# Kernel tuning notes

Measured on AMD Instinct MI355X. Metric: run time of the kernel, lower is better.

Reference implementation:

```python
import jax, jax.numpy as jnp
import numpy as np

B, N, DEG = 32, 1024, 8
E = B * N * DEG
NT = B * N
F_IN, HID, EDIM, NR, HD = 64, 128, 16, 16, 4
NEG = 0.2  # leaky_relu negative slope (alpha)
K1 = int(np.ceil(0.8 * N))    # 820 kept nodes per graph after pool1
K2 = int(np.ceil(0.8 * K1))   # 656 kept nodes per graph after pool2


def setup_inputs() -> dict:
    key = jax.random.key(0)
    ks = jax.random.split(key, 20)
    nrm = lambda i, shp, s=0.05: jax.random.normal(ks[i], shp, jnp.float32) * s
    x = jax.random.normal(ks[0], (NT, F_IN), jnp.float32)
    off = (jnp.arange(B) * N)[:, None]
    src = (jax.random.randint(ks[1], (B, N * DEG), 0, N) + off).reshape(-1)
    dst = (jax.random.randint(ks[2], (B, N * DEG), 0, N) + off).reshape(-1)
    edge_index = jnp.stack([src, dst]).astype(jnp.int32)
    edge_attr = jax.random.normal(ks[3], (E, EDIM), jnp.float32)
    action = jax.random.normal(ks[4], (B, NR), jnp.float32)
    return dict(
        x=x, edge_attr=edge_attr, action=action,
        W1l=nrm(5, (F_IN, HD * HID)), b1l=jnp.zeros(HD * HID),
        W1r=nrm(6, (F_IN, HD * HID)), b1r=jnp.zeros(HD * HID),
        W1e=nrm(7, (EDIM, HD * HID)), att1=nrm(8, (HD, HID)), bias1=jnp.zeros(HID),
        W2l=nrm(9, (HID, HD * HID)), b2l=jnp.zeros(HD * HID),
        W2r=nrm(10, (HID, HD * HID)), b2r=jnp.zeros(HD * HID),
        W2e=nrm(11, (EDIM, HD * HID)), att2=nrm(12, (HD, HID)), bias2=jnp.zeros(HID),
        p1=nrm(13, (HID,), 0.1), p2=nrm(14, (HID,), 0.1),
        Wf1=nrm(15, (2 * HID + NR, HID)), bf1=jnp.zeros(HID),
        Wf2=nrm(16, (HID, HID)), bf2=jnp.zeros(HID),
        Wf3=nrm(17, (HID, 1), 0.003), bf3=jnp.zeros(1),
        edge_index=edge_index,
    )


def _gatv2(x, edge_index, edge_attr, edge_mask, Wl, bl, Wr, br, We, att, bias):
    # PyG GATv2Conv, concat=False (mean over heads), eval mode (no dropout).
    src, dst = edge_index[0], edge_index[1]
    n = x.shape[0]
    xl = (x @ Wl + bl).reshape(n, HD, HID)   # source transform (x_j)
    xr = (x @ Wr + br).reshape(n, HD, HID)   # target transform (x_i)
    ef = (edge_attr @ We).reshape(-1, HD, HID)
    m = jax.nn.leaky_relu(xl[src] + xr[dst] + ef, NEG)          # [E,H,C]
    logits = jnp.where(edge_mask[:, None], (m * att).sum(-1), -1e9)  # [E,H]
    mx = jax.ops.segment_max(logits, dst, num_segments=n)
    a = jnp.exp(logits - mx[dst])
    den = jax.ops.segment_sum(a, dst, num_segments=n)
    alpha = (a / (den[dst] + 1e-16)) * edge_mask[:, None]       # softmax per dst, masked edges zeroed
    out = jax.ops.segment_sum(xl[src] * alpha[..., None], dst, num_segments=n)
    return out.mean(axis=1) + bias


def _topk(x, node_mask, p, k):
    # PyG TopKPooling: score = x@p/||p||, gate = tanh(score), keep top-k per graph.
    score = (x @ p) / (jnp.linalg.norm(p) + 1e-16)
    gate = jnp.tanh(score)
    s = jnp.where(node_mask, score, -jnp.inf).reshape(B, N)
    idx = jax.lax.top_k(s, k)[1]                                # [B,k]
    keep = jnp.zeros((B, N), bool).at[jnp.arange(B)[:, None], idx].set(True).reshape(-1)
    return x * gate[:, None], keep


def reference(x, edge_attr, action, W1l, b1l, W1r, b1r, W1e, att1, bias1,
              W2l, b2l, W2r, b2r, W2e, att2, bias2, p1, p2,
              Wf1, bf1, Wf2, bf2, Wf3, bf3, edge_index):
    src, dst = edge_index[0], edge_index[1]
    em0 = jnp.ones((E,), bool)
    h = jax.nn.relu(_gatv2(x, edge_index, edge_attr, em0,
                           W1l, b1l, W1r, b1r, W1e, att1, bias1))
    h, keep1 = _topk(h, jnp.ones((NT,), bool), p1, K1)
    em1 = keep1[src] & keep1[dst]
    h = jax.nn.relu(_gatv2(h, edge_index, edge_attr, em1,
                           W2l, b2l, W2r, b2r, W2e, att2, bias2))
    h, keep2 = _topk(h, keep1, p2, K2)
    hb = h.reshape(B, N, HID)
    mb = keep2.reshape(B, N)[..., None]
    gmx = jnp.where(mb, hb, -jnp.inf).max(axis=1)               # global max pool over kept nodes
    gav = (hb * mb).sum(axis=1) / K2                            # global mean pool (K2 kept per graph)
    z = jnp.concatenate([gmx, gav, action], axis=1)             # [B, 2*HID+NR]
    z = jax.nn.relu(z @ Wf1 + bf1)
    z = jax.nn.relu(z @ Wf2 + bf2)
    return z @ Wf3 + bf3
```

## Files before the change

kernel.cpp:

```cpp
#include <hip/hip_runtime.h>
#include <math.h>

#define NTN 32768
#define NBG 32
#define NN  1024
#define EPG 8192
#define EE  262144
#define FIN 64
#define HIDC 128
#define HD  4
#define HC  512
#define EDIM 16
#define NR  16
#define KP1 820
#define KP2 656
#define NKEPT (KP1 * NBG)
#define NEGS 0.2f
#define NPB 2
#define SHIFT 10.0f

template<int K>
__global__ __launch_bounds__(256) void gemm_node3(const float* __restrict__ A,
                                                  const float* __restrict__ Wl,
                                                  const float* __restrict__ bl,
                                                  const float* __restrict__ Wr,
                                                  const float* __restrict__ br,
                                                  const float* __restrict__ gs,
                                                  const int* __restrict__ ids,
                                                  float* __restrict__ Cl,
                                                  float* __restrict__ Cr,
                                                  const int* __restrict__ perm,
                                                  const float* __restrict__ ea,
                                                  float* __restrict__ eaP) {
    __shared__ float a_s[64][K];
    __shared__ int rid_s[64];
    __shared__ float g_s[64];
    int t = threadIdx.x;
    int rb = blockIdx.x >> 2, cg = blockIdx.x & 3;
    int row0 = rb * 64;
    if (t < 64) {
        int rid = ids ? ids[row0 + t] : (row0 + t);
        rid_s[t] = rid;
        g_s[t] = gs ? tanhf(gs[rid]) : 1.0f;
    }
    __syncthreads();
    for (int i = t; i < 64 * K; i += 256) {
        int r = i / K, k = i % K;
        a_s[r][k] = A[(size_t)rid_s[r] * K + k] * g_s[r];
    }
    __syncthreads();
    int tc = cg * 128 + (t & 63) * 2;
    int rg = (t >> 6) * 16;
    float accl0[16], accl1[16], accr0[16], accr1[16];
    float2 blv = *(const float2*)&bl[tc];
    float2 brv = *(const float2*)&br[tc];
    #pragma unroll
    for (int r = 0; r < 16; r++) { accl0[r] = blv.x; accl1[r] = blv.y; accr0[r] = brv.x; accr1[r] = brv.y; }
    for (int k = 0; k < K; k++) {
        float2 wl = *(const float2*)&Wl[(size_t)k * HC + tc];
        float2 wr = *(const float2*)&Wr[(size_t)k * HC + tc];
        #pragma unroll
        for (int r = 0; r < 16; r++) {
            float a = a_s[rg + r][k];
            accl0[r] += a * wl.x; accl1[r] += a * wl.y;
            accr0[r] += a * wr.x; accr1[r] += a * wr.y;
        }
    }
    for (int r = 0; r < 16; r++) {
        size_t base = (size_t)rid_s[rg + r] * HC + tc;
        *(float2*)&Cl[base] = make_float2(accl0[r], accl1[r]);
        *(float2*)&Cr[base] = make_float2(accr0[r], accr1[r]);
    }
    if (perm) {
        int ng = gridDim.x * 256;
        for (int p = blockIdx.x * 256 + t; p < EE; p += ng) {
            int e = perm[p];
            const float4* s4 = (const float4*)(ea + (size_t)e * EDIM);
            float4* d4 = (float4*)(eaP + (size_t)p * EDIM);
            d4[0] = s4[0]; d4[1] = s4[1]; d4[2] = s4[2]; d4[3] = s4[3];
        }
    }
}

__global__ __launch_bounds__(1024) void csr_build(const int* __restrict__ dst,
                                                  const int* __restrict__ src,
                                                  int* __restrict__ off,
                                                  int* __restrict__ esrc,
                                                  int* __restrict__ perm,
                                                  const float* __restrict__ p1,
                                                  const float* __restrict__ p2,
                                                  float* __restrict__ pn) {
    int g = blockIdx.x, t = threadIdx.x;
    __shared__ int degS[NN];
    __shared__ int scanS[NN];
    __shared__ int curS[NN];
    degS[t] = 0;
    __syncthreads();
    int eb = g * EPG;
    #pragma unroll
    for (int i = t; i < EPG; i += 1024) atomicAdd(&degS[dst[eb + i] - g * NN], 1);
    __syncthreads();
    int dg = degS[t];
    scanS[t] = dg;
    for (int o = 1; o < NN; o <<= 1) {
        __syncthreads();
        int v = (t >= o) ? scanS[t - o] : 0;
        __syncthreads();
        scanS[t] += v;
    }
    __syncthreads();
    int excl = scanS[t] - dg;
    off[g * NN + t] = eb + excl;
    curS[t] = excl;
    if (g == NBG - 1 && t == NN - 1) off[NTN] = EE;
    if (g == 0 && t < 64) {
        float a = p1[t] * p1[t] + p1[t + 64] * p1[t + 64];
        float b = p2[t] * p2[t] + p2[t + 64] * p2[t + 64];
        #pragma unroll
        for (int sft = 32; sft; sft >>= 1) { a += __shfl_xor(a, sft, 64); b += __shfl_xor(b, sft, 64); }
        if (t == 0) { pn[0] = 1.f / (sqrtf(a) + 1e-16f); pn[1] = 1.f / (sqrtf(b) + 1e-16f); }
    }
    __syncthreads();
    #pragma unroll
    for (int i = t; i < EPG; i += 1024) {
        int e = eb + i;
        int ld = dst[e] - g * NN;
        int p = eb + atomicAdd(&curS[ld], 1);
        esrc[p] = src[e];
        perm[p] = e;
    }
}

template<bool L2>
__global__ __launch_bounds__(256, 4) void gat_dst(
        const float* __restrict__ xl, const float* __restrict__ xr,
        const float* __restrict__ eaP, const float* __restrict__ We,
        const float* __restrict__ att, const float* __restrict__ bias,
        const float* __restrict__ pvec, const float* __restrict__ pnInv,
        const int* __restrict__ esrc, const int* __restrict__ off,
        const int* __restrict__ dlist,
        float* __restrict__ out, float* __restrict__ score, int nblk) {
    int bid = blockIdx.x;
    int swz = (bid & 7) * (nblk >> 3) + (bid >> 3);
    int d0 = swz * NPB;
    int t = threadIdx.x;
    int w = t >> 6, lane = t & 63;
    int c = w * HIDC + lane * 2;
    __shared__ float red[NPB][HC];
    __shared__ float red2[NPB][HIDC];
    float we0[EDIM], we1[EDIM];
    #pragma unroll
    for (int k = 0; k < EDIM; k++) {
        we0[k] = We[k * HC + c];
        we1[k] = We[k * HC + c + 1];
    }
    float at0 = att[c], at1 = att[c + 1];

    for (int n = 0; n < NPB; n++) {
        int d = L2 ? dlist[d0 + n] : (d0 + n);
        float denA = 0.f, aA0 = 0.f, aA1 = 0.f;
        float denB = 0.f, aB0 = 0.f, aB1 = 0.f;
        {
            float2 xrv = *(const float2*)&xr[((size_t)d << 9) + c];
            int e0 = off[d], e1 = off[d + 1];
            int ei = e0;
            for (; ei + 4 <= e1; ei += 4) {
                int s[4]; float mk[4]; float2 xv[4]; float p[4];
                #pragma unroll
                for (int j = 0; j < 4; j++) {
                    int sv = esrc[ei + j];
                    if (L2) {
                        mk[j] = sv >= 0 ? 1.f : 0.f;
                        s[j] = sv >= 0 ? sv : 0;
                    } else {
                        s[j] = sv;
                    }
                }
                #pragma unroll
                for (int j = 0; j < 4; j++) xv[j] = *(const float2*)&xl[((size_t)s[j] << 9) + c];
                #pragma unroll
                for (int j = 0; j < 4; j++) {
                    const float4* eap = (const float4*)(eaP + ((size_t)(ei + j) << 4));
                    float4 E0 = eap[0], E1 = eap[1], E2 = eap[2], E3 = eap[3];
                    float ev[16] = {E0.x, E0.y, E0.z, E0.w, E1.x, E1.y, E1.z, E1.w,
                                    E2.x, E2.y, E2.z, E2.w, E3.x, E3.y, E3.z, E3.w};
                    float ef0 = 0.f, ef1 = 0.f;
                    #pragma unroll
                    for (int k = 0; k < EDIM; k++) { ef0 += ev[k] * we0[k]; ef1 += ev[k] * we1[k]; }
                    float v0 = xv[j].x + xrv.x + ef0; v0 = v0 > 0.f ? v0 : NEGS * v0;
                    float v1 = xv[j].y + xrv.y + ef1; v1 = v1 > 0.f ? v1 : NEGS * v1;
                    p[j] = v0 * at0 + v1 * at1;
                }
                #pragma unroll
                for (int sft = 32; sft; sft >>= 1) {
                    #pragma unroll
                    for (int j = 0; j < 4; j++) p[j] += __shfl_xor(p[j], sft, 64);
                }
                float w0 = __expf(p[0] - SHIFT);
                float w1 = __expf(p[1] - SHIFT);
                float w2 = __expf(p[2] - SHIFT);
                float w3 = __expf(p[3] - SHIFT);
                if (L2) { w0 *= mk[0]; w1 *= mk[1]; w2 *= mk[2]; w3 *= mk[3]; }
                denA += w0; aA0 += w0 * xv[0].x; aA1 += w0 * xv[0].y;
                denB += w1; aB0 += w1 * xv[1].x; aB1 += w1 * xv[1].y;
                denA += w2; aA0 += w2 * xv[2].x; aA1 += w2 * xv[2].y;
                denB += w3; aB0 += w3 * xv[3].x; aB1 += w3 * xv[3].y;
            }
            for (; ei < e1; ei++) {
                int sv = esrc[ei];
                float mk = 1.f;
                int s = sv;
                if (L2) { mk = sv >= 0 ? 1.f : 0.f; s = sv >= 0 ? sv : 0; }
                const float4* eap = (const float4*)(eaP + ((size_t)ei << 4));
                float4 E0 = eap[0], E1 = eap[1], E2 = eap[2], E3 = eap[3];
                float2 xv = *(const float2*)&xl[((size_t)s << 9) + c];
                float ev[16] = {E0.x, E0.y, E0.z, E0.w, E1.x, E1.y, E1.z, E1.w,
                                E2.x, E2.y, E2.z, E2.w, E3.x, E3.y, E3.z, E3.w};
                float ef0 = 0.f, ef1 = 0.f;
                #pragma unroll
                for (int k = 0; k < EDIM; k++) { ef0 += ev[k] * we0[k]; ef1 += ev[k] * we1[k]; }
                float v0 = xv.x + xrv.x + ef0; v0 = v0 > 0.f ? v0 : NEGS * v0;
                float v1 = xv.y + xrv.y + ef1; v1 = v1 > 0.f ? v1 : NEGS * v1;
                float p = v0 * at0 + v1 * at1;
                #pragma unroll
                for (int sft = 32; sft; sft >>= 1) p += __shfl_xor(p, sft, 64);
                float wt = __expf(p - SHIFT);
                if (L2) wt *= mk;
                denA += wt; aA0 += wt * xv.x; aA1 += wt * xv.y;
            }
        }
        float inv = 1.f / (denA + denB + 1e-16f);
        red[n][c] = (aA0 + aB0) * inv;
        red[n][c + 1] = (aA1 + aB1) * inv;
    }
    __syncthreads();
    {
        int n2 = t >> 7, tc = t & 127;
        int dd = L2 ? dlist[d0 + n2] : (d0 + n2);
        float v = (red[n2][tc] + red[n2][tc + 128] + red[n2][tc + 256] + red[n2][tc + 384]) * 0.25f
                  + bias[tc];
        v = fmaxf(v, 0.f);
        out[((size_t)dd << 7) + tc] = v;
        red2[n2][tc] = v * pvec[tc];
    }
    __syncthreads();
    if (t < 128) {
        int n3 = t >> 6, l2 = t & 63;
        float sv = red2[n3][l2] + red2[n3][l2 + 64];
        #pragma unroll
        for (int sft = 32; sft; sft >>= 1) sv += __shfl_xor(sv, sft, 64);
        if (l2 == 0) {
            int dd = L2 ? dlist[d0 + n3] : (d0 + n3);
            score[dd] = sv * pnInv[0];
        }
    }
}

__global__ __launch_bounds__(512) void topk_sel(const float* __restrict__ score,
                                                const int* __restrict__ mask, int k,
                                                int* __restrict__ keep, int* __restrict__ klist,
                                                const int* __restrict__ esrc,
                                                int* __restrict__ esrc2) {
    __shared__ float v[NN];
    __shared__ short id[NN];
    __shared__ char kpS[NN];
    int g = blockIdx.x, t = threadIdx.x;
    for (int i = t; i < NN; i += 512) {
        int n = g * NN + i;
        bool mk = mask ? (mask[n] != 0) : true;
        v[i] = mk ? score[n] : -INFINITY;
        id[i] = (short)i;
    }
    __syncthreads();
    for (int kk = 2; kk <= NN; kk <<= 1) {
        for (int j = kk >> 1; j > 0; j >>= 1) {
            #pragma unroll 2
            for (int i = t; i < NN; i += 512) {
                int ixj = i ^ j;
                if (ixj > i) {
                    bool up = ((i & kk) == 0);
                    float a = v[i], b2 = v[ixj];
                    short ia = id[i], ib = id[ixj];
                    bool aFirst = (a > b2) || (a == b2 && ia < ib);
                    if (up ? !aFirst : aFirst) { v[i] = b2; v[ixj] = a; id[i] = ib; id[ixj] = ia; }
                }
            }
            __syncthreads();
        }
    }
    for (int i = t; i < NN; i += 512) {
        int kp = (i < k) ? 1 : 0;
        keep[g * NN + id[i]] = kp;
        kpS[id[i]] = (char)kp;
        if (klist && kp) klist[g * k + i] = g * NN + id[i];
    }
    __syncthreads();
    if (esrc2) {
        int eb = g * EPG;
        for (int i = t; i < EPG; i += 512) {
            int sv = esrc[eb + i];
            esrc2[eb + i] = kpS[sv - g * NN] ? sv : -1;
        }
    }
}

__global__ __launch_bounds__(512) void tail(const float* __restrict__ score,
                                            const int* __restrict__ mask,
                                            const float* __restrict__ h,
                                            const float* __restrict__ action,
                                            const float* __restrict__ Wf1, const float* __restrict__ bf1,
                                            const float* __restrict__ Wf2, const float* __restrict__ bf2,
                                            const float* __restrict__ Wf3, const float* __restrict__ bf3,
                                            float* __restrict__ out) {
    int g = blockIdx.x, t = threadIdx.x;
    __shared__ float v[NN];
    __shared__ short id[NN];
    __shared__ float gt_s[NN];
    __shared__ char kp_s[NN];
    __shared__ float smx[4][HIDC], ssm[4][HIDC];
    __shared__ float zs[2 * HIDC + NR], z1[HIDC], z2[HIDC], rr[HIDC];
    for (int i = t; i < NN; i += 512) {
        int n = g * NN + i;
        bool mk = (mask[n] != 0);
        v[i] = mk ? score[n] : -INFINITY;
        id[i] = (short)i;
        kp_s[i] = 0;
        gt_s[i] = 0.f;
    }
    __syncthreads();
    for (int kk = 2; kk <= NN; kk <<= 1) {
        for (int j = kk >> 1; j > 0; j >>= 1) {
            #pragma unroll 2
            for (int i = t; i < NN; i += 512) {
                int ixj = i ^ j;
                if (ixj > i) {
                    bool up = ((i & kk) == 0);
                    float a = v[i], b2 = v[ixj];
                    short ia = id[i], ib = id[ixj];
                    bool aFirst = (a > b2) || (a == b2 && ia < ib);
                    if (up ? !aFirst : aFirst) { v[i] = b2; v[ixj] = a; id[i] = ib; id[ixj] = ia; }
                }
            }
            __syncthreads();
        }
    }
    for (int i = t; i < NN; i += 512) {
        if (i < KP2) {
            int nid = id[i];
            kp_s[nid] = 1;
            gt_s[nid] = tanhf(score[g * NN + nid]);
        }
    }
    __syncthreads();
    int c = t & 127, ch = t >> 7;
    float mx = -INFINITY, sm = 0.f;
    for (int n = ch * 256; n < ch * 256 + 256; n++) {
        if (kp_s[n]) {
            float hv = h[(size_t)(g * NN + n) * HIDC + c] * gt_s[n];
            mx = fmaxf(mx, hv);
            sm += hv;
        }
    }
    smx[ch][c] = mx; ssm[ch][c] = sm;
    __syncthreads();
    if (t < HIDC) {
        mx = fmaxf(fmaxf(smx[0][t], smx[1][t]), fmaxf(smx[2][t], smx[3][t]));
        sm = ssm[0][t] + ssm[1][t] + ssm[2][t] + ssm[3][t];
        zs[t] = mx;
        zs[HIDC + t] = sm / (float)KP2;
        if (t < NR) zs[2 * HIDC + t] = action[g * NR + t];
    }
    __syncthreads();
    if (t < HIDC) {
        float a = bf1[t];
        for (int k = 0; k < 2 * HIDC + NR; k++) a += zs[k] * Wf1[(size_t)k * HIDC + t];
        z1[t] = fmaxf(a, 0.f);
    }
    __syncthreads();
    if (t < HIDC) {
        float a = bf2[t];
        for (int k = 0; k < HIDC; k++) a += z1[k] * Wf2[(size_t)k * HIDC + t];
        z2[t] = fmaxf(a, 0.f);
        rr[t] = z2[t] * Wf3[t];
    }
    __syncthreads();
    for (int s = 64; s; s >>= 1) {
        if (t < s) rr[t] += rr[t + s];
        __syncthreads();
    }
    if (t == 0) out[g] = rr[0] + bf3[0];
}

extern "C" void kernel_launch(void* const* d_in, const int* in_sizes, int n_in,
                              void* d_out, int out_size, void* d_ws, size_t ws_size,
                              hipStream_t stream) {
    const float* x    = (const float*)d_in[0];
    const float* ea   = (const float*)d_in[1];
    const float* act  = (const float*)d_in[2];
    const float* W1l  = (const float*)d_in[3];
    const float* b1l  = (const float*)d_in[4];
    const float* W1r  = (const float*)d_in[5];
    const float* b1r  = (const float*)d_in[6];
    const float* W1e  = (const float*)d_in[7];
    const float* att1 = (const float*)d_in[8];
    const float* bias1= (const float*)d_in[9];
    const float* W2l  = (const float*)d_in[10];
    const float* b2l  = (const float*)d_in[11];
    const float* W2r  = (const float*)d_in[12];
    const float* b2r  = (const float*)d_in[13];
    const float* W2e  = (const float*)d_in[14];
    const float* att2 = (const float*)d_in[15];
    const float* bias2= (const float*)d_in[16];
    const float* p1   = (const float*)d_in[17];
    const float* p2   = (const float*)d_in[18];
    const float* Wf1  = (const float*)d_in[19];
    const float* bf1  = (const float*)d_in[20];
    const float* Wf2  = (const float*)d_in[21];
    const float* bf2  = (const float*)d_in[22];
    const float* Wf3  = (const float*)d_in[23];
    const float* bf3  = (const float*)d_in[24];
    const int*   eix  = (const int*)d_in[25];
    const int* srcA = eix;
    const int* dstA = eix + EE;

    float* ws    = (float*)d_ws;
    float* xl    = ws;
    float* xr    = xl + (size_t)NTN * HC;
    float* h     = xr + (size_t)NTN * HC;
    float* score1= h + (size_t)NTN * HIDC;
    float* score2= score1 + NTN;
    float* pn    = score2 + NTN;
    int* keep1 = (int*)(pn + 2);
    int* klist = keep1 + NTN;
    int* off   = klist + NKEPT;
    int* esrc  = off + NTN + 1;
    int* esrc2 = esrc + EE;
    int* perm  = esrc2 + EE;
    float* eaP = (float*)(perm + EE);

    csr_build<<<NBG, 1024, 0, stream>>>(dstA, srcA, off, esrc, perm, p1, p2, pn);

    gemm_node3<FIN><<<(NTN / 64) * 4, 256, 0, stream>>>(x, W1l, b1l, W1r, b1r, nullptr, nullptr,
                                                        xl, xr, perm, ea, eaP);
    gat_dst<false><<<NTN / NPB, 256, 0, stream>>>(xl, xr, eaP, W1e, att1, bias1, p1, pn, esrc, off,
                                                  nullptr, h, score1, NTN / NPB);

    topk_sel<<<NBG, 512, 0, stream>>>(score1, nullptr, KP1, keep1, klist, esrc, esrc2);

    gemm_node3<HIDC><<<(NKEPT / 64) * 4, 256, 0, stream>>>(h, W2l, b2l, W2r, b2r, score1, klist,
                                                           xl, xr, nullptr, nullptr, nullptr);
    gat_dst<true><<<NKEPT / NPB, 256, 0, stream>>>(xl, xr, eaP, W2e, att2, bias2, p2, pn + 1, esrc2, off,
                                                   klist, h, score2, NKEPT / NPB);

    tail<<<NBG, 512, 0, stream>>>(score2, keep1, h, act,
                                  Wf1, bf1, Wf2, bf2, Wf3, bf3, (float*)d_out);
}
```

Before: 525.8 us.

## Enlarge gemm row tiles and stream edge weights instead of holding them in registers

The node GEMM now processes 128 rows per 512-thread block instead of 64 per 256, halving the block count and reusing each loaded weight across more rows. The GAT kernel no longer keeps the 32 edge-weight values in registers; it reloads them from global/cache on every edge, which cuts register pressure so more waves can stay resident. The edge loop is unrolled by 2 instead of 4, reducing in-flight registers but also the number of gathers issued together. The risks are the extra repeated We loads and less memory-level parallelism per wave. NKEPT/128 = 205 whole tiles, so the grid stays valid.

```diff
diff --git a/kernel.cpp b/kernel.cpp
--- a/kernel.cpp
+++ b/kernel.cpp
@@ -20,7 +20,7 @@
 #define SHIFT 10.0f
 
 template<int K>
-__global__ __launch_bounds__(256) void gemm_node3(const float* __restrict__ A,
+__global__ __launch_bounds__(512) void gemm_node3(const float* __restrict__ A,
                                                   const float* __restrict__ Wl,
                                                   const float* __restrict__ bl,
                                                   const float* __restrict__ Wr,
@@ -32,19 +32,19 @@
                                                   const int* __restrict__ perm,
                                                   const float* __restrict__ ea,
                                                   float* __restrict__ eaP) {
-    __shared__ float a_s[64][K];
-    __shared__ int rid_s[64];
-    __shared__ float g_s[64];
+    __shared__ float a_s[128][K];
+    __shared__ int rid_s[128];
+    __shared__ float g_s[128];
     int t = threadIdx.x;
     int rb = blockIdx.x >> 2, cg = blockIdx.x & 3;
-    int row0 = rb * 64;
-    if (t < 64) {
+    int row0 = rb * 128;
+    if (t < 128) {
         int rid = ids ? ids[row0 + t] : (row0 + t);
         rid_s[t] = rid;
         g_s[t] = gs ? tanhf(gs[rid]) : 1.0f;
     }
     __syncthreads();
-    for (int i = t; i < 64 * K; i += 256) {
+    for (int i = t; i < 128 * K; i += 512) {
         int r = i / K, k = i % K;
         a_s[r][k] = A[(size_t)rid_s[r] * K + k] * g_s[r];
     }
@@ -72,8 +72,8 @@
         *(float2*)&Cr[base] = make_float2(accr0[r], accr1[r]);
     }
     if (perm) {
-        int ng = gridDim.x * 256;
-        for (int p = blockIdx.x * 256 + t; p < EE; p += ng) {
+        int ng = gridDim.x * 512;
+        for (int p = blockIdx.x * 512 + t; p < EE; p += ng) {
             int e = perm[p];
             const float4* s4 = (const float4*)(ea + (size_t)e * EDIM);
             float4* d4 = (float4*)(eaP + (size_t)p * EDIM);
@@ -148,13 +148,28 @@
     int c = w * HIDC + lane * 2;
     __shared__ float red[NPB][HC];
     __shared__ float red2[NPB][HIDC];
-    float we0[EDIM], we1[EDIM];
-    #pragma unroll
-    for (int k = 0; k < EDIM; k++) {
-        we0[k] = We[k * HC + c];
-        we1[k] = We[k * HC + c + 1];
-    }
     float at0 = att[c], at1 = att[c + 1];
+
+#define DOT4P(Ea, Eb, kb)                                                        \
+    {                                                                            \
+        float2 w0v = *(const float2*)&We[(kb + 0) * HC + c];                     \
+        float2 w1v = *(const float2*)&We[(kb + 1) * HC + c];                     \
+        float2 w2v = *(const float2*)&We[(kb + 2) * HC + c];                     \
+        float2 w3v = *(const float2*)&We[(kb + 3) * HC + c];                     \
+        ef00 += Ea.x * w0v.x + Ea.y * w1v.x + Ea.z * w2v.x + Ea.w * w3v.x;       \
+        ef01 += Ea.x * w0v.y + Ea.y * w1v.y + Ea.z * w2v.y + Ea.w * w3v.y;       \
+        ef10 += Eb.x * w0v.x + Eb.y * w1v.x + Eb.z * w2v.x + Eb.w * w3v.x;       \
+        ef11 += Eb.x * w0v.y + Eb.y * w1v.y + Eb.z * w2v.y + Eb.w * w3v.y;       \
+    }
+#define DOT4S(Ea, kb)                                                            \
+    {                                                                            \
+        float2 w0v = *(const float2*)&We[(kb + 0) * HC + c];                     \
+        float2 w1v = *(const float2*)&We[(kb + 1) * HC + c];                     \
+        float2 w2v = *(const float2*)&We[(kb + 2) * HC + c];                     \
+        float2 w3v = *(const float2*)&We[(kb + 3) * HC + c];                     \
+        ef00 += Ea.x * w0v.x + Ea.y * w1v.x + Ea.z * w2v.x + Ea.w * w3v.x;       \
+        ef01 += Ea.x * w0v.y + Ea.y * w1v.y + Ea.z * w2v.y + Ea.w * w3v.y;       \
+    }
 
     for (int n = 0; n < NPB; n++) {
         int d = L2 ? dlist[d0 + n] : (d0 + n);
@@ -164,63 +179,56 @@
             float2 xrv = *(const float2*)&xr[((size_t)d << 9) + c];
             int e0 = off[d], e1 = off[d + 1];
             int ei = e0;
-            for (; ei + 4 <= e1; ei += 4) {
-                int s[4]; float mk[4]; float2 xv[4]; float p[4];
-                #pragma unroll
-                for (int j = 0; j < 4; j++) {
-                    int sv = esrc[ei + j];
-                    if (L2) {
-                        mk[j] = sv >= 0 ? 1.f : 0.f;
-                        s[j] = sv >= 0 ? sv : 0;
-                    } else {
-                        s[j] = sv;
-                    }
+            for (; ei + 2 <= e1; ei += 2) {
+                int sv0 = esrc[ei], sv1 = esrc[ei + 1];
+                float mk0 = 1.f, mk1 = 1.f;
+                int s0 = sv0, s1 = sv1;
+                if (L2) {
+                    mk0 = sv0 >= 0 ? 1.f : 0.f; s0 = sv0 >= 0 ? sv0 : 0;
+                    mk1 = sv1 >= 0 ? 1.f : 0.f; s1 = sv1 >= 0 ? sv1 : 0;
                 }
-                #pragma unroll
-                for (int j = 0; j < 4; j++) xv[j] = *(const float2*)&xl[((size_t)s[j] << 9) + c];
-                #pragma unroll
-                for (int j = 0; j < 4; j++) {
-                    const float4* eap = (const float4*)(eaP + ((size_t)(ei + j) << 4));
-                    float4 E0 = eap[0], E1 = eap[1], E2 = eap[2], E3 = eap[3];
-                    float ev[16] = {E0.x, E0.y, E0.z, E0.w, E1.x, E1.y, E1.z, E1.w,
-                                    E2.x, E2.y, E2.z, E2.w, E3.x, E3.y, E3.z, E3.w};
-                    float ef0 = 0.f, ef1 = 0.f;
-                    #pragma unroll
-                    for (int k = 0; k < EDIM; k++) { ef0 += ev[k] * we0[k]; ef1 += ev[k] * we1[k]; }
-                    float v0 = xv[j].x + xrv.x + ef0; v0 = v0 > 0.f ? v0 : NEGS * v0;
-                    float v1 = xv[j].y + xrv.y + ef1; v1 = v1 > 0.f ? v1 : NEGS * v1;
-                    p[j] = v0 * at0 + v1 * at1;
-                }
+                float2 xv0 = *(const float2*)&xl[((size_t)s0 << 9) + c];
+                float2 xv1 = *(const float2*)&xl[((size_t)s1 << 9) + c];
+                const float4* eap = (const float4*)(eaP + ((size_t)ei << 4));
+                float4 A0 = eap[0], A1 = eap[1], A2 = eap[2], A3 = eap[3];
+                float4 B0 = eap[4], B1 = eap[5], B2 = eap[6], B3 = eap[7];
+                float ef00 = 0.f, ef01 = 0.f, ef10 = 0.f, ef11 = 0.f;
+                DOT4P(A0, B0, 0);
+                DOT4P(A1, B1, 4);
+                DOT4P(A2, B2, 8);
+                DOT4P(A3, B3, 12);
+                float v00 = xv0.x + xrv.x + ef00; v00 = v00 > 0.f ? v00 : NEGS * v00;
+                float v01 = xv0.y + xrv.y + ef01; v01 = v01 > 0.f ? v01 : NEGS * v01;
+                float v10 = xv1.x + xrv.x + ef10; v10 = v10 > 0.f ? v10 : NEGS * v10;
+                float v11 = xv1.y + xrv.y + ef11; v11 = v11 > 0.f ? v11 : NEGS * v11;
+                float p0 = v00 * at0 + v01 * at1;
+                float p1 = v10 * at0 + v11 * at1;
                 #pragma unroll
                 for (int sft = 32; sft; sft >>= 1) {
-                    #pragma unroll
-                    for (int j = 0; j < 4; j++) p[j] += __shfl_xor(p[j], sft, 64);
+                    p0 += __shfl_xor(p0, sft, 64);
+                    p1 += __shfl_xor(p1, sft, 64);
                 }
-                float w0 = __expf(p[0] - SHIFT);
-                float w1 = __expf(p[1] - SHIFT);
-                float w2 = __expf(p[2] - SHIFT);
-                float w3 = __expf(p[3] - SHIFT);
-                if (L2) { w0 *= mk[0]; w1 *= mk[1]; w2 *= mk[2]; w3 *= mk[3]; }
-                denA += w0; aA0 += w0 * xv[0].x; aA1 += w0 * xv[0].y;
-                denB += w1; aB0 += w1 * xv[1].x; aB1 += w1 * xv[1].y;
-                denA += w2; aA0 += w2 * xv[2].x; aA1 += w2 * xv[2].y;
-                denB += w3; aB0 += w3 * xv[3].x; aB1 += w3 * xv[3].y;
+                float w0 = __expf(p0 - SHIFT);
+                float w1 = __expf(p1 - SHIFT);
+                if (L2) { w0 *= mk0; w1 *= mk1; }
+                denA += w0; aA0 += w0 * xv0.x; aA1 += w0 * xv0.y;
+                denB += w1; aB0 += w1 * xv1.x; aB1 += w1 * xv1.y;
             }
-            for (; ei < e1; ei++) {
+            if (ei < e1) {
                 int sv = esrc[ei];
                 float mk = 1.f;
                 int s = sv;
                 if (L2) { mk = sv >= 0 ? 1.f : 0.f; s = sv >= 0 ? sv : 0; }
+                float2 xv = *(const float2*)&xl[((size_t)s << 9) + c];
                 const float4* eap = (const float4*)(eaP + ((size_t)ei << 4));
-                float4 E0 = eap[0], E1 = eap[1], E2 = eap[2], E3 = eap[3];
-                float2 xv = *(const float2*)&xl[((size_t)s << 9) + c];
-                float ev[16] = {E0.x, E0.y, E0.z, E0.w, E1.x, E1.y, E1.z, E1.w,
-                                E2.x, E2.y, E2.z, E2.w, E3.x, E3.y, E3.z, E3.w};
-                float ef0 = 0.f, ef1 = 0.f;
-                #pragma unroll
-                for (int k = 0; k < EDIM; k++) { ef0 += ev[k] * we0[k]; ef1 += ev[k] * we1[k]; }
-                float v0 = xv.x + xrv.x + ef0; v0 = v0 > 0.f ? v0 : NEGS * v0;
-                float v1 = xv.y + xrv.y + ef1; v1 = v1 > 0.f ? v1 : NEGS * v1;
+                float4 A0 = eap[0], A1 = eap[1], A2 = eap[2], A3 = eap[3];
+                float ef00 = 0.f, ef01 = 0.f;
+                DOT4S(A0, 0);
+                DOT4S(A1, 4);
+                DOT4S(A2, 8);
+                DOT4S(A3, 12);
+                float v0 = xv.x + xrv.x + ef00; v0 = v0 > 0.f ? v0 : NEGS * v0;
+                float v1 = xv.y + xrv.y + ef01; v1 = v1 > 0.f ? v1 : NEGS * v1;
                 float p = v0 * at0 + v1 * at1;
                 #pragma unroll
                 for (int sft = 32; sft; sft >>= 1) p += __shfl_xor(p, sft, 64);
@@ -233,6 +241,8 @@
         red[n][c] = (aA0 + aB0) * inv;
         red[n][c + 1] = (aA1 + aB1) * inv;
     }
+#undef DOT4P
+#undef DOT4S
     __syncthreads();
     {
         int n2 = t >> 7, tc = t & 127;
@@ -440,15 +450,15 @@
 
     csr_build<<<NBG, 1024, 0, stream>>>(dstA, srcA, off, esrc, perm, p1, p2, pn);
 
-    gemm_node3<FIN><<<(NTN / 64) * 4, 256, 0, stream>>>(x, W1l, b1l, W1r, b1r, nullptr, nullptr,
-                                                        xl, xr, perm, ea, eaP);
+    gemm_node3<FIN><<<(NTN / 128) * 4, 512, 0, stream>>>(x, W1l, b1l, W1r, b1r, nullptr, nullptr,
+                                                         xl, xr, perm, ea, eaP);
     gat_dst<false><<<NTN / NPB, 256, 0, stream>>>(xl, xr, eaP, W1e, att1, bias1, p1, pn, esrc, off,
                                                   nullptr, h, score1, NTN / NPB);
 
     topk_sel<<<NBG, 512, 0, stream>>>(score1, nullptr, KP1, keep1, klist, esrc, esrc2);
 
-    gemm_node3<HIDC><<<(NKEPT / 64) * 4, 256, 0, stream>>>(h, W2l, b2l, W2r, b2r, score1, klist,
-                                                           xl, xr, nullptr, nullptr, nullptr);
+    gemm_node3<HIDC><<<(NKEPT / 128) * 4, 512, 0, stream>>>(h, W2l, b2l, W2r, b2r, score1, klist,
+                                                            xl, xr, nullptr, nullptr, nullptr);
     gat_dst<true><<<NKEPT / NPB, 256, 0, stream>>>(xl, xr, eaP, W2e, att2, bias2, p2, pn + 1, esrc2, off,
                                                    klist, h, score2, NKEPT / NPB);
 
```

Measured after the change: 644.6 us. +22.6%, slower.
